# Performance work log

Measured on AMD Instinct MI355X. Metric: run time of the kernel, lower is better.

The kernel has to match this reference:

```python
import jax, jax.numpy as jnp
import numpy as np

D_MODEL = 1024
NUM_HEADS = 16
HEAD_DIM = D_MODEL // NUM_HEADS


def setup_inputs() -> dict:
    key = jax.random.key(0)
    k_x, k_wqkv, k_bqkv, k_wfc, k_bfc = jax.random.split(key, 5)
    scale_in = 1.0 / np.sqrt(D_MODEL)
    return {
        "x": jax.random.normal(k_x, (2, 2048, D_MODEL), dtype=jnp.float32),
        # torch nn.Linear stores weight as [out_features, in_features]
        "w_qkv": jax.random.uniform(k_wqkv, (3 * D_MODEL, D_MODEL), jnp.float32, -scale_in, scale_in),
        "b_qkv": jax.random.uniform(k_bqkv, (3 * D_MODEL,), jnp.float32, -scale_in, scale_in),
        "w_fc": jax.random.uniform(k_wfc, (D_MODEL, D_MODEL), jnp.float32, -scale_in, scale_in),
        "b_fc": jax.random.uniform(k_bfc, (D_MODEL,), jnp.float32, -scale_in, scale_in),
    }


def reference(x, w_qkv, b_qkv, w_fc, b_fc):
    B, S, _ = x.shape
    # fused QKV projection: [B,S,3*d_model]
    qkv = jnp.einsum("bsd,ed->bse", x, w_qkv) + b_qkv
    # [B,S,H,3*head_dim] -> [B,H,S,3*head_dim]
    qkv = qkv.reshape(B, S, NUM_HEADS, 3 * HEAD_DIM).transpose(0, 2, 1, 3)
    Q, K, V = jnp.split(qkv, 3, axis=-1)  # each [B,H,S,head_dim]
    scores = jnp.einsum("bhqd,bhkd->bhqk", Q, K) / np.sqrt(HEAD_DIM).astype(np.float32)
    attention = jax.nn.softmax(scores, axis=-1)  # [B,H,S,S]
    values = jnp.einsum("bhqk,bhkd->bhqd", attention, V)
    # [B,H,S,head_dim] -> [B,S,d_model]
    values = values.transpose(0, 2, 1, 3).reshape(B, S, D_MODEL)
    out = jnp.einsum("bsd,ed->bse", values, w_fc) + b_fc
    return out
```

## Files before the change

kernel.cpp:

```cpp
#include <hip/hip_runtime.h>
#include <hip/hip_bf16.h>
#include <hip/hip_fp16.h>

#define D_MODEL 1024
#define NH 16
#define HD 64
#define BATCH 2
#define SEQ 2048

typedef __attribute__((ext_vector_type(8))) short short8;
typedef __attribute__((ext_vector_type(4))) float floatx4;
typedef __attribute__((ext_vector_type(16))) float floatx16;
typedef __attribute__((ext_vector_type(8))) _Float16 half8;

static __device__ __forceinline__ short f2bf(float f) {
    __hip_bfloat16 h = __float2bfloat16(f);
    return *reinterpret_cast<short*>(&h);
}
static __device__ __forceinline__ unsigned int pk2bf(float a, float b) {
    float2 t; t.x = a; t.y = b;
    __hip_bfloat162 h2 = __float22bfloat162_rn(t);
    return *reinterpret_cast<unsigned int*>(&h2);
}
static __device__ __forceinline__ void pl32swap(unsigned &a, unsigned &b) {
    asm("v_permlane32_swap_b32 %0, %1" : "+v"(a), "+v"(b));
}
static __device__ __forceinline__ short8 mk8(unsigned a, unsigned b,
                                             unsigned c, unsigned d) {
    union { unsigned u[4]; short8 s; } t;
    t.u[0] = a; t.u[1] = b; t.u[2] = c; t.u[3] = d;
    return t.s;
}

#define GLDS(gp, lp) __builtin_amdgcn_global_load_lds( \
    (const __attribute__((address_space(1))) void*)(gp), \
    (__attribute__((address_space(3))) void*)(lp), 16, 0, 0)

__global__ __launch_bounds__(256) void cvt_all(
    const float* __restrict__ x, const float* __restrict__ wq,
    const float* __restrict__ wf,
    short* __restrict__ Xb, short* __restrict__ Wqb, short* __restrict__ Wfb)
{
    int i = blockIdx.x * 256 + threadIdx.x;
    const float* src; short* dst; int off;
    if (i < 524288)      { src = x;  dst = Xb;  off = i; }
    else if (i < 917504) { src = wq; dst = Wqb; off = i - 524288; }
    else                 { src = wf; dst = Wfb; off = i - 917504; }
    float4 a = *reinterpret_cast<const float4*>(src + off * 8);
    float4 b = *reinterpret_cast<const float4*>(src + off * 8 + 4);
    short8 o;
    o[0] = f2bf(a.x); o[1] = f2bf(a.y); o[2] = f2bf(a.z); o[3] = f2bf(a.w);
    o[4] = f2bf(b.x); o[5] = f2bf(b.y); o[6] = f2bf(b.z); o[7] = f2bf(b.w);
    *reinterpret_cast<short8*>(dst + off * 8) = o;
}

__global__ __launch_bounds__(256) void qkv_gemm(
    const short* __restrict__ X, const short* __restrict__ W,
    const float* __restrict__ bias,
    short* __restrict__ Qs, short* __restrict__ Ks, short* __restrict__ Vt_g)
{
    __shared__ __align__(16) short SH[2][128 * 64];
    short* As = &SH[0][0];
    short* Bs = &SH[1][0];
    const int tid = threadIdx.x;

    const int lin = blockIdx.x;
    const int g = lin & 7;
    const int loc = lin >> 3;
    const int mi = loc / 3;
    const int j3 = loc - mi * 3;
    const int m0 = mi * 128;
    const int n0 = (g + 8 * j3) * 128;
    const int bi = m0 >> 11, sl0 = m0 & 2047;

    const int w = tid >> 6, lane = tid & 63;
    const int quad = lane >> 4, l15 = lane & 15;
    const int wm2 = w >> 1, wn2 = w & 1;

    const int rg = lane >> 3;
    const int sl = lane & 7;
    const int cg = sl ^ rg;

    floatx4 acc[4][4];
#pragma unroll
    for (int i = 0; i < 4; i++)
#pragma unroll
        for (int j = 0; j < 4; j++) acc[i][j] = (floatx4)0.0f;

    for (int k0 = 0; k0 < 1024; k0 += 64) {
        __syncthreads();
#pragma unroll
        for (int jj = 0; jj < 4; jj++) {
            int grp = w * 4 + jj;
            int r = grp * 8 + rg;
            GLDS(&X[(size_t)(m0 + r) * 1024 + k0 + cg * 8], &As[grp * 512]);
            GLDS(&W[(size_t)(n0 + r) * 1024 + k0 + cg * 8], &Bs[grp * 512]);
        }
        __syncthreads();
#pragma unroll
        for (int kk = 0; kk < 2; kk++) {
            const int ch = kk * 4 + quad;
            short8 a[4], b[4];
#pragma unroll
            for (int t = 0; t < 4; t++) {
                int ra = wm2 * 64 + t * 16 + l15;
                int rb = wn2 * 64 + t * 16 + l15;
                a[t] = *reinterpret_cast<const short8*>(
                    &As[(ra >> 3) * 512 + (ra & 7) * 64 + ((ch ^ (ra & 7)) * 8)]);
                b[t] = *reinterpret_cast<const short8*>(
                    &Bs[(rb >> 3) * 512 + (rb & 7) * 64 + ((ch ^ (rb & 7)) * 8)]);
            }
#pragma unroll
            for (int mt = 0; mt < 4; mt++)
#pragma unroll
                for (int nt = 0; nt < 4; nt++)
                    acc[mt][nt] = __builtin_amdgcn_mfma_f32_16x16x32_bf16(
                        a[mt], b[nt], acc[mt][nt], 0, 0, 0);
        }
    }

    __syncthreads();
    short* EA = &SH[0][0];
    short* T  = &SH[0][0];
#pragma unroll
    for (int half = 0; half < 2; half++) {
        const int colg0 = n0 + half * 64;
        const int h = colg0 / 192;
        const int t = (colg0 % 192) / 64;
        if (wn2 == half) {
#pragma unroll
            for (int nt = 0; nt < 4; nt++) {
                int jj = nt * 16 + l15;
                float bv = bias[colg0 + jj];
#pragma unroll
                for (int mt = 0; mt < 4; mt++) {
#pragma unroll
                    for (int r = 0; r < 4; r++) {
                        int ml = wm2 * 64 + mt * 16 + quad * 4 + r;
                        float v = acc[mt][nt][r] + bv;
                        if (t == 0) v *= 0.18033688f;
                        if (t < 2) EA[ml * 72 + jj] = f2bf(v);
                        else       T[jj * 136 + ml] = f2bf(v);
                    }
                }
            }
        }
        __syncthreads();
        if (t < 2) {
            short* dst = (t == 0) ? Qs : Ks;
#pragma unroll
            for (int i = 0; i < 4; i++) {
                int c = tid + i * 256;
                int row = c >> 3, ck = c & 7;
                uint4 u = *reinterpret_cast<const uint4*>(&EA[row * 72 + ck * 8]);
                *reinterpret_cast<uint4*>(
                    &dst[((size_t)(bi * NH + h) * SEQ + sl0 + row) * HD + ck * 8]) = u;
            }
        } else {
#pragma unroll
            for (int i = 0; i < 4; i++) {
                int c = tid + i * 256;
                int d = c >> 4, ck = c & 15;
                uint4 u = *reinterpret_cast<const uint4*>(&T[d * 136 + ck * 8]);
                *reinterpret_cast<uint4*>(
                    &Vt_g[((size_t)(bi * NH + h) * HD + d) * SEQ + sl0 + ck * 8]) = u;
            }
        }
        __syncthreads();
    }
}

__global__ __launch_bounds__(512, 4) void attn_kernel(
    const short* __restrict__ Qs, const short* __restrict__ Ks,
    const short* __restrict__ Vt_g,
    _Float16* __restrict__ Opart, float* __restrict__ lpart)
{
    __shared__ __align__(16) short Kl[2][32 * 64];
    __shared__ __align__(16) short Vl[2][32 * 64];

    const int tid = threadIdx.x;
    const int w = tid >> 6;
    const int lane = tid & 63;
    const int hi = lane >> 5, l31 = lane & 31;

    const int lin = blockIdx.x;
    const int xcd = lin & 7;
    const int j = lin >> 3;
    const int qb = j & 7;
    const int grp = xcd + 8 * (j >> 3);
    const int khalf = grp & 1;
    const int h = (grp >> 1) & 15;
    const int bi = grp >> 5;
    const int bh = bi * NH + h;
    const int kbase = bh * SEQ * HD;
    const int vbase = bh * HD * SEQ;
    const int kt0 = khalf * (SEQ / 2);
    const int qw = qb * 256 + w * 32;

    const int st = tid & 255;
    const int sr = st >> 3;
    const int ss = st & 7;
    const int cgs = ss ^ (sr & 7);
    const short* kg = Ks + kbase + (size_t)(kt0 + sr) * HD + cgs * 8;
    const short* vg = Vt_g + vbase +
                      (size_t)(sr + (cgs >> 2) * 32) * SEQ + kt0 + (cgs & 3) * 8;

    short8 aq[4];
    {
        const short* qp = Qs + kbase + (size_t)(qw + l31) * HD + hi * 8;
#pragma unroll
        for (int c = 0; c < 4; c++)
            aq[c] = *reinterpret_cast<const short8*>(qp + c * 16);
    }

    floatx16 o0 = (floatx16)0.0f, o1 = (floatx16)0.0f;
    float l_acc = 0.0f;

    const int rbase = (l31 >> 3) * 512 + (l31 & 7) * 64;
    const int rx = l31 & 7;

    if (tid < 256) GLDS(kg, &Kl[0][st * 8]);
    else           GLDS(vg, &Vl[0][st * 8]);
    __syncthreads();

    int cur = 0;
    for (int it = 0; it < SEQ / 2 / 32; it++) {
        if (tid < 256) GLDS(kg + (size_t)(it + 1) * (32 * HD), &Kl[cur ^ 1][st * 8]);
        else           GLDS(vg + (it + 1) * 32, &Vl[cur ^ 1][st * 8]);

        const short* Kb = &Kl[cur][0];
        const short* Vb = &Vl[cur][0];
        short8 kf[4], vA0, vA1, vB0, vB1;
#pragma unroll
        for (int c = 0; c < 4; c++)
            kf[c] = *reinterpret_cast<const short8*>(
                Kb + rbase + (((2 * c + hi) ^ rx) * 8));
        vA0 = *reinterpret_cast<const short8*>(Vb + rbase + (((0 + hi) ^ rx) * 8));
        vA1 = *reinterpret_cast<const short8*>(Vb + rbase + (((2 + hi) ^ rx) * 8));
        vB0 = *reinterpret_cast<const short8*>(Vb + rbase + (((4 + hi) ^ rx) * 8));
        vB1 = *reinterpret_cast<const short8*>(Vb + rbase + (((6 + hi) ^ rx) * 8));

        floatx16 s = (floatx16)0.0f;
        s = __builtin_amdgcn_mfma_f32_32x32x16_bf16(kf[0], aq[0], s, 0, 0, 0);
        s = __builtin_amdgcn_mfma_f32_32x32x16_bf16(kf[1], aq[1], s, 0, 0, 0);
        s = __builtin_amdgcn_mfma_f32_32x32x16_bf16(kf[2], aq[2], s, 0, 0, 0);
        s = __builtin_amdgcn_mfma_f32_32x32x16_bf16(kf[3], aq[3], s, 0, 0, 0);

        float p[16];
#pragma unroll
        for (int r = 0; r < 16; r++) p[r] = exp2f(s[r]);

        {
            float s0 = (p[0] + p[1]) + (p[2] + p[3]);
            float s1 = (p[4] + p[5]) + (p[6] + p[7]);
            float s2 = (p[8] + p[9]) + (p[10] + p[11]);
            float s3 = (p[12] + p[13]) + (p[14] + p[15]);
            l_acc += (s0 + s1) + (s2 + s3);
        }

        unsigned d0a = pk2bf(p[0], p[1]),   d2a = pk2bf(p[4], p[5]);
        unsigned d1a = pk2bf(p[2], p[3]),   d3a = pk2bf(p[6], p[7]);
        pl32swap(d0a, d2a);
        pl32swap(d1a, d3a);
        unsigned d0b = pk2bf(p[8], p[9]),   d2b = pk2bf(p[12], p[13]);
        unsigned d1b = pk2bf(p[10], p[11]), d3b = pk2bf(p[14], p[15]);
        pl32swap(d0b, d2b);
        pl32swap(d1b, d3b);
        short8 pa0 = mk8(d0a, d1a, d2a, d3a);
        short8 pa1 = mk8(d0b, d1b, d2b, d3b);

        o0 = __builtin_amdgcn_mfma_f32_32x32x16_bf16(pa0, vA0, o0, 0, 0, 0);
        o1 = __builtin_amdgcn_mfma_f32_32x32x16_bf16(pa0, vB0, o1, 0, 0, 0);
        o0 = __builtin_amdgcn_mfma_f32_32x32x16_bf16(pa1, vA1, o0, 0, 0, 0);
        o1 = __builtin_amdgcn_mfma_f32_32x32x16_bf16(pa1, vB1, o1, 0, 0, 0);

        __syncthreads();
        cur ^= 1;
    }

#pragma unroll
    for (int r = 0; r < 16; r++) {
        int ql = qw + (r & 3) + 8 * (r >> 2) + 4 * hi;
        size_t base = (size_t)khalf * (4096u * 1024u) +
                      ((size_t)bi * SEQ + ql) * D_MODEL + h * HD;
        Opart[base + l31]      = (_Float16)o0[r];
        Opart[base + 32 + l31] = (_Float16)o1[r];
    }
    float l_oth = __shfl_xor(l_acc, 32);
    if (hi == 0)
        lpart[khalf * 65536 + bh * SEQ + qw + l31] = l_acc + l_oth;
}

__global__ __launch_bounds__(256) void combine_kernel(
    const _Float16* __restrict__ O, const float* __restrict__ lp,
    short* __restrict__ attnb)
{
    int i = blockIdx.x * 256 + threadIdx.x;
    int m = i >> 7;
    int e0 = (i & 127) * 8;
    int bi = m >> 11, s = m & 2047, h = e0 >> 6;
    int bh = bi * NH + h;
    float l = lp[bh * SEQ + s] + lp[65536 + bh * SEQ + s];
    float rl = 1.0f / l;
    size_t off = (size_t)m * D_MODEL + e0;
    half8 a = *reinterpret_cast<const half8*>(O + off);
    half8 b = *reinterpret_cast<const half8*>(O + 4096u * 1024u + off);
    short8 out;
#pragma unroll
    for (int j = 0; j < 8; j++)
        out[j] = f2bf(((float)a[j] + (float)b[j]) * rl);
    *reinterpret_cast<short8*>(attnb + off) = out;
}

__global__ __launch_bounds__(256) void fc_gemm(
    const short* __restrict__ A, const short* __restrict__ W,
    const float* __restrict__ bias, float* __restrict__ out)
{
    __shared__ __align__(16) short As[128 * 64];
    __shared__ __align__(16) short Bs[64 * 64];
    const int tid = threadIdx.x;
    const int m0 = blockIdx.y * 128;
    const int n0 = blockIdx.x * 64;
    const int w = tid >> 6, lane = tid & 63;
    const int quad = lane >> 4, l15 = lane & 15;
    const int wm2 = w >> 1, wn2 = w & 1;

    const int rg = lane >> 3;
    const int sl = lane & 7;
    const int cg = sl ^ rg;

    floatx4 acc[4][2];
#pragma unroll
    for (int i = 0; i < 4; i++)
#pragma unroll
        for (int j = 0; j < 2; j++) acc[i][j] = (floatx4)0.0f;

    for (int k0 = 0; k0 < 1024; k0 += 64) {
        __syncthreads();
#pragma unroll
        for (int j = 0; j < 4; j++) {
            int g = w * 4 + j;
            int r = g * 8 + rg;
            GLDS(&A[(size_t)(m0 + r) * 1024 + k0 + cg * 8], &As[g * 512]);
        }
#pragma unroll
        for (int j = 0; j < 2; j++) {
            int g = w * 2 + j;
            int r = g * 8 + rg;
            GLDS(&W[(size_t)(n0 + r) * 1024 + k0 + cg * 8], &Bs[g * 512]);
        }
        __syncthreads();
#pragma unroll
        for (int kk = 0; kk < 2; kk++) {
            int swz = ((kk * 4 + quad) ^ (l15 & 7)) * 8;
            short8 a[4], b[2];
#pragma unroll
            for (int i = 0; i < 4; i++)
                a[i] = *reinterpret_cast<const short8*>(
                    &As[(wm2 * 64 + i * 16 + l15) * 64 + swz]);
#pragma unroll
            for (int j = 0; j < 2; j++)
                b[j] = *reinterpret_cast<const short8*>(
                    &Bs[(wn2 * 32 + j * 16 + l15) * 64 + swz]);
#pragma unroll
            for (int mt = 0; mt < 4; mt++)
#pragma unroll
                for (int nt = 0; nt < 2; nt++)
                    acc[mt][nt] = __builtin_amdgcn_mfma_f32_16x16x32_bf16(
                        a[mt], b[nt], acc[mt][nt], 0, 0, 0);
        }
    }

#pragma unroll
    for (int nt = 0; nt < 2; nt++) {
        int col = n0 + wn2 * 32 + nt * 16 + l15;
        float bv = bias[col];
#pragma unroll
        for (int mt = 0; mt < 4; mt++) {
#pragma unroll
            for (int r = 0; r < 4; r++) {
                int row = m0 + wm2 * 64 + mt * 16 + quad * 4 + r;
                out[row * 1024 + col] = acc[mt][nt][r] + bv;
            }
        }
    }
}

extern "C" void kernel_launch(void* const* d_in, const int* in_sizes, int n_in,
                              void* d_out, int out_size, void* d_ws, size_t ws_size,
                              hipStream_t stream) {
    const float* x     = (const float*)d_in[0];
    const float* w_qkv = (const float*)d_in[1];
    const float* b_qkv = (const float*)d_in[2];
    const float* w_fc  = (const float*)d_in[3];
    const float* b_fc  = (const float*)d_in[4];
    float* out = (float*)d_out;

    const size_t M1 = 1024u * 1024u;
    short* ws = (short*)d_ws;
    short* Qs    = ws;
    short* Ks    = ws + 4 * M1;
    short* Vt_g  = ws + 8 * M1;
    short* Wfb   = ws + 12 * M1;
    short* Xb    = ws + 13 * M1;
    short* Wqb   = ws + 17 * M1;
    _Float16* Opart = (_Float16*)(ws + 13 * M1);
    float* lpart = (float*)(ws + 21 * M1);
    short* attnb = Qs;

    cvt_all<<<4096, 256, 0, stream>>>(x, w_qkv, w_fc, Xb, Wqb, Wfb);
    qkv_gemm<<<768, 256, 0, stream>>>(Xb, Wqb, b_qkv, Qs, Ks, Vt_g);
    attn_kernel<<<512, 512, 0, stream>>>(Qs, Ks, Vt_g, Opart, lpart);
    combine_kernel<<<2048, 256, 0, stream>>>(Opart, lpart, attnb);
    fc_gemm<<<dim3(16, 32), 256, 0, stream>>>(attnb, Wfb, b_fc, out);
}
```

Baseline: 213.8 us.

## Double-buffer QKV GEMM LDS tiles with K=32 steps and prefetch

The QKV projection GEMM now splits LDS into two ping-pong buffers per operand with a K-step of 32. It issues the async global-to-LDS loads for the next tile before the MFMAs on the current one, and needs only one barrier per step instead of two. The LDS swizzle is redone for the 32-wide rows. In exchange there are twice as many K-iterations. The final prefetch also reads one tile past the end of each row, which can touch memory beyond the last row's buffer.

```diff
diff --git a/kernel.cpp b/kernel.cpp
--- a/kernel.cpp
+++ b/kernel.cpp
@@ -59,9 +59,7 @@
     const float* __restrict__ bias,
     short* __restrict__ Qs, short* __restrict__ Ks, short* __restrict__ Vt_g)
 {
-    __shared__ __align__(16) short SH[2][128 * 64];
-    short* As = &SH[0][0];
-    short* Bs = &SH[1][0];
+    __shared__ __align__(16) short SH[4][128 * 32];
     const int tid = threadIdx.x;
 
     const int lin = blockIdx.x;
@@ -77,9 +75,17 @@
     const int quad = lane >> 4, l15 = lane & 15;
     const int wm2 = w >> 1, wn2 = w & 1;
 
-    const int rg = lane >> 3;
-    const int sl = lane & 7;
-    const int cg = sl ^ rg;
+    const int r1 = tid >> 2,        c1 = tid & 3;
+    const int g1 = c1 ^ (r1 & 3) ^ ((r1 >> 2) & 3);
+    const int r2 = (tid + 256) >> 2, c2 = tid & 3;
+    const int g2 = c2 ^ (r2 & 3) ^ ((r2 >> 2) & 3);
+
+    const short* Xs1 = X + (size_t)(m0 + r1) * 1024 + g1 * 8;
+    const short* Xs2 = X + (size_t)(m0 + r2) * 1024 + g2 * 8;
+    const short* Ws1 = W + (size_t)(n0 + r1) * 1024 + g1 * 8;
+    const short* Ws2 = W + (size_t)(n0 + r2) * 1024 + g2 * 8;
+
+    const int rsw = (quad ^ (l15 & 3) ^ ((l15 >> 2) & 3)) * 8;
 
     floatx4 acc[4][4];
 #pragma unroll
@@ -87,36 +93,39 @@
 #pragma unroll
         for (int j = 0; j < 4; j++) acc[i][j] = (floatx4)0.0f;
 
-    for (int k0 = 0; k0 < 1024; k0 += 64) {
-        __syncthreads();
-#pragma unroll
-        for (int jj = 0; jj < 4; jj++) {
-            int grp = w * 4 + jj;
-            int r = grp * 8 + rg;
-            GLDS(&X[(size_t)(m0 + r) * 1024 + k0 + cg * 8], &As[grp * 512]);
-            GLDS(&W[(size_t)(n0 + r) * 1024 + k0 + cg * 8], &Bs[grp * 512]);
-        }
-        __syncthreads();
-#pragma unroll
-        for (int kk = 0; kk < 2; kk++) {
-            const int ch = kk * 4 + quad;
-            short8 a[4], b[4];
-#pragma unroll
-            for (int t = 0; t < 4; t++) {
-                int ra = wm2 * 64 + t * 16 + l15;
-                int rb = wn2 * 64 + t * 16 + l15;
-                a[t] = *reinterpret_cast<const short8*>(
-                    &As[(ra >> 3) * 512 + (ra & 7) * 64 + ((ch ^ (ra & 7)) * 8)]);
-                b[t] = *reinterpret_cast<const short8*>(
-                    &Bs[(rb >> 3) * 512 + (rb & 7) * 64 + ((ch ^ (rb & 7)) * 8)]);
-            }
-#pragma unroll
-            for (int mt = 0; mt < 4; mt++)
-#pragma unroll
-                for (int nt = 0; nt < 4; nt++)
-                    acc[mt][nt] = __builtin_amdgcn_mfma_f32_16x16x32_bf16(
-                        a[mt], b[nt], acc[mt][nt], 0, 0, 0);
-        }
+    GLDS(Xs1, &SH[0][tid * 8]);
+    GLDS(Xs2, &SH[0][(tid + 256) * 8]);
+    GLDS(Ws1, &SH[2][tid * 8]);
+    GLDS(Ws2, &SH[2][(tid + 256) * 8]);
+    __syncthreads();
+
+    int cur = 0;
+    for (int step = 0; step < 32; step++) {
+        const int kn = (step + 1) * 32;
+        GLDS(Xs1 + kn, &SH[cur ^ 1][tid * 8]);
+        GLDS(Xs2 + kn, &SH[cur ^ 1][(tid + 256) * 8]);
+        GLDS(Ws1 + kn, &SH[2 + (cur ^ 1)][tid * 8]);
+        GLDS(Ws2 + kn, &SH[2 + (cur ^ 1)][(tid + 256) * 8]);
+
+        const short* As = &SH[cur][0];
+        const short* Bs = &SH[2 + cur][0];
+        short8 a[4], b[4];
+#pragma unroll
+        for (int t = 0; t < 4; t++) {
+            int ra = wm2 * 64 + t * 16 + l15;
+            int rb = wn2 * 64 + t * 16 + l15;
+            a[t] = *reinterpret_cast<const short8*>(&As[ra * 32 + rsw]);
+            b[t] = *reinterpret_cast<const short8*>(&Bs[rb * 32 + rsw]);
+        }
+#pragma unroll
+        for (int mt = 0; mt < 4; mt++)
+#pragma unroll
+            for (int nt = 0; nt < 4; nt++)
+                acc[mt][nt] = __builtin_amdgcn_mfma_f32_16x16x32_bf16(
+                    a[mt], b[nt], acc[mt][nt], 0, 0, 0);
+
+        __syncthreads();
+        cur ^= 1;
     }
 
     __syncthreads();
```

Result: faster. 199.8 us (-6.5%).
